# Optimization experiments

Measured on AMD Instinct MI355X. Metric: run time of the kernel, lower is better.

The kernel has to match this reference:

```python
import jax, jax.numpy as jnp
import numpy as np

B, CIN, COUT, H, W = 8, 128, 128, 64, 64

# kernel-grid base offsets (dy, dx), row-major k = kh*3 + kw, matching torch base_offset-1
BASE = jnp.array([[-1, -1], [-1, 0], [-1, 1],
                  [0, -1], [0, 0], [0, 1],
                  [1, -1], [1, 0], [1, 1]], dtype=jnp.float32)  # [9,2]
CORNER = jnp.array([1, 0, 1, 0, 0, 0, 1, 0, 1], dtype=jnp.float32)  # mask1 per kernel tap
EDGE = jnp.array([0, 1, 0, 1, 0, 1, 0, 1, 0], dtype=jnp.float32)    # mask2 per kernel tap


def conv3x3(x, w, b=None):
    out = jax.lax.conv_general_dilated(
        x, w, window_strides=(1, 1), padding=((1, 1), (1, 1)),
        dimension_numbers=('NCHW', 'OIHW', 'NCHW'))
    if b is not None:
        out = out + b[None, :, None, None]
    return out


def bilinear_sample(x, py, px):
    Bv, C, Hin, Win = x.shape
    y0 = jnp.floor(py)
    x0 = jnp.floor(px)
    wy = py - y0
    wx = px - x0
    y0i = y0.astype(jnp.int32)
    x0i = x0.astype(jnp.int32)
    xf = x.reshape(Bv, C, Hin * Win)

    def corner(yi, xi):
        valid = ((yi >= 0) & (yi < Hin) & (xi >= 0) & (xi < Win)).astype(x.dtype)
        idx = jnp.clip(yi, 0, Hin - 1) * Win + jnp.clip(xi, 0, Win - 1)  # [B,K,Ho,Wo]
        g = jax.vmap(lambda xb, ib: xb[:, ib])(xf, idx)  # [B,C,K,Ho,Wo]
        return g * valid[:, None]

    v00 = corner(y0i, x0i)
    v01 = corner(y0i, x0i + 1)
    v10 = corner(y0i + 1, x0i)
    v11 = corner(y0i + 1, x0i + 1)
    wy = wy[:, None]
    wx = wx[:, None]
    return (v00 * (1 - wy) * (1 - wx) + v01 * (1 - wy) * wx
            + v10 * wy * (1 - wx) + v11 * wy * wx)


def setup_inputs() -> dict:
    key = jax.random.key(0)
    k1, k2, k3 = jax.random.split(key, 3)
    x = jax.random.normal(k1, (B, CIN, H, W), dtype=jnp.float32)
    # small offset-conv weights keep predicted offsets in a realistic sub-pixel range
    w_off = jax.random.normal(k2, (5, CIN, 3, 3), dtype=jnp.float32) * 0.02
    b_off = jnp.zeros((5,), dtype=jnp.float32)
    w = jax.random.normal(k3, (COUT, CIN, 3, 3), dtype=jnp.float32) * (1.0 / np.sqrt(CIN * 9))
    b = jnp.zeros((COUT,), dtype=jnp.float32)
    return {"x": x, "w_off": w_off, "b_off": b_off, "w": w, "b": b}


def reference(x, w_off, b_off, w, b):
    off = conv3x3(x, w_off, b_off)          # [B,5,H,W]
    scale1 = jax.nn.relu(off[:, 2:3]) + 1.0  # corner scale [B,1,H,W]
    scale2 = jax.nn.relu(off[:, 3:4]) + 1.0  # edge scale   [B,1,H,W]
    shift = off[:, :2]                       # equivariant shift vector [B,2,H,W]

    # per-tap scale; center tap gets 0 but its base offset is (0,0) anyway
    scale_k = CORNER[None, :, None, None] * scale1 + EDGE[None, :, None, None] * scale2  # [B,9,H,W]
    # deform offset = scaled_base - base + shift = base*(scale-1) + shift
    delta = BASE[None, :, :, None, None] * (scale_k - 1.0)[:, :, None] + shift[:, None]  # [B,9,2,H,W]

    hs = jnp.arange(H, dtype=x.dtype)
    ws = jnp.arange(W, dtype=x.dtype)
    # sampling positions: p0 + base_k + offset_k (stride=1, pad=1)
    py = hs[None, None, :, None] + BASE[None, :, 0, None, None] + delta[:, :, 0]  # [B,9,H,W]
    px = ws[None, None, None, :] + BASE[None, :, 1, None, None] + delta[:, :, 1]

    sampled = bilinear_sample(x, py, px)  # [B,CIN,9,H,W]
    out = jnp.einsum('bckhw,ock->bohw', sampled, w.reshape(COUT, CIN, 9))
    return out + b[None, :, None, None]
```

## Files before the change

kernel.cpp:

```cpp
#include <hip/hip_runtime.h>

#define Wd 64
#define Hd 64
#define HWp 4096
#define CIN_ 128
#define COUT_ 128

typedef _Float16 f16;
typedef _Float16 h2    __attribute__((ext_vector_type(2)));
typedef _Float16 f16x8 __attribute__((ext_vector_type(8)));
typedef float f32x4    __attribute__((ext_vector_type(4)));

__device__ inline ushort f2h(float f) {
    f16 h = (f16)f;
    return __builtin_bit_cast(ushort, h);
}
__device__ inline h2 gb(const int4& g, int d) {
    return __builtin_bit_cast(h2, (&g.x)[d]);
}
__device__ inline h2 dup(float f) {
    f16 h = (f16)f;
    h2 r; r[0] = h; r[1] = h;
    return r;
}
struct H8 { h2 r[4]; };

__global__ __launch_bounds__(512) void prep_offsets_kernel(
    const float* __restrict__ x, const float* __restrict__ w,
    const float* __restrict__ w_off, const float* __restrict__ b_off,
    ushort* __restrict__ xt, ushort* __restrict__ w_t2,
    float4* __restrict__ der)
{
    __shared__ char smem[43520];
    int blk = blockIdx.x;
    int t = threadIdx.x;

    if (blk < 40) {
        int i8 = blk * 512 + t;
        if (i8 < 18432) {
            int lane = i8 & 63;
            int ii   = (i8 >> 6) & 3;
            int wm   = (i8 >> 8) & 1;
            int s    = i8 >> 9;
            int o  = wm * 64 + ii * 16 + (lane & 15);
            int cb = (s & 3) * 32 + (lane >> 4) * 8;
            int k  = s >> 2;
            ushort tmp[8];
            #pragma unroll
            for (int j = 0; j < 8; j++)
                tmp[j] = f2h(w[o * 1152 + (cb + j) * 9 + k]);
            *(int4*)&w_t2[(size_t)i8 * 8] = *(int4*)tmp;
        }
    } else {
        float* wl    = (float*)smem;
        float* part  = (float*)(smem + 18432);
        ushort* tile = (ushort*)(smem + 26624);
        int blk2 = blk - 40;
        int b = blk2 & 7;
        int h = blk2 >> 3;

        for (int i = t; i < 4608; i += 512) {
            int j = i / 1152;
            int r = i - j * 1152;
            wl[r * 4 + j] = w_off[i];
        }
        __syncthreads();

        int pi = t & 63, cg = t >> 6;
        const float* xb = x + (size_t)(b * CIN_ + cg * 16) * HWp;

        int idxc[3];
        float mskl[3], mskc[3], mskr[3];
        #pragma unroll
        for (int dy = 0; dy < 3; dy++) {
            int hy = h + dy - 1;
            int hyc = min(max(hy, 0), Hd - 1);
            bool vr = (hy >= 0) && (hy < Hd);
            idxc[dy] = hyc * Wd + pi;
            mskc[dy] = vr ? 1.0f : 0.0f;
            mskl[dy] = (vr && pi > 0) ? 1.0f : 0.0f;
            mskr[dy] = (vr && pi < Wd - 1) ? 1.0f : 0.0f;
        }

        float o0 = 0.f, o1 = 0.f, o2 = 0.f, o3 = 0.f;
        #pragma unroll
        for (int c4 = 0; c4 < 4; c4++) {
            ushort4 hv;
            #pragma unroll
            for (int j = 0; j < 4; j++) {
                int c = c4 * 4 + j;
                const float* xp = xb + c * HWp;
                const float* wc = &wl[(cg * 16 + c) * 36];
                float xv[9];
                #pragma unroll
                for (int dy = 0; dy < 3; dy++) {
                    float v = xp[idxc[dy]];
                    xv[dy * 3 + 0] = __shfl_up(v, 1) * mskl[dy];
                    xv[dy * 3 + 1] = v * mskc[dy];
                    xv[dy * 3 + 2] = __shfl_down(v, 1) * mskr[dy];
                }
                (&hv.x)[j] = f2h(xv[4]);
                #pragma unroll
                for (int tp = 0; tp < 9; tp++) {
                    float4 wj = *(const float4*)&wc[tp * 4];
                    o0 += xv[tp] * wj.x; o1 += xv[tp] * wj.y;
                    o2 += xv[tp] * wj.z; o3 += xv[tp] * wj.w;
                }
            }
            *(ushort4*)&tile[pi * 132 + cg * 16 + c4 * 4] = hv;
        }
        part[t * 4 + 0] = o0;
        part[t * 4 + 1] = o1;
        part[t * 4 + 2] = o2;
        part[t * 4 + 3] = o3;
        __syncthreads();

        {
            ushort* dst = xt + ((size_t)b * HWp + h * 64) * CIN_;
            #pragma unroll
            for (int k = 0; k < 2; k++) {
                int q = t + k * 512;
                int row = q >> 4, c16 = q & 15;
                int4 v = *(const int4*)&tile[row * 132 + c16 * 8];
                *(int4*)(dst + q * 8) = v;
            }
        }

        if (t < 64) {
            float s0 = b_off[0], s1 = b_off[1], s2 = b_off[2], s3 = b_off[3];
            #pragma unroll
            for (int q = 0; q < 8; q++) {
                s0 += part[(q * 64 + t) * 4 + 0];
                s1 += part[(q * 64 + t) * 4 + 1];
                s2 += part[(q * 64 + t) * 4 + 2];
                s3 += part[(q * 64 + t) * 4 + 3];
            }
            float4 d;
            d.x = s0;
            d.y = s1;
            d.z = fmaxf(s2, 0.f) + 1.f;
            d.w = fmaxf(s3, 0.f) + 1.f;
            der[(size_t)b * HWp + h * Wd + t] = d;
        }
    }
}

__global__ __launch_bounds__(256, 2) void deform_gemm_mfma(
    const ushort* __restrict__ xt, const ushort* __restrict__ w_t2,
    const float* __restrict__ bias, const float4* __restrict__ der,
    float* __restrict__ out)
{
    __shared__ ushort A_lds[2][2][4096];
    __shared__ ushort S_lds[2][2][64 * 40];
    __shared__ int4 MI[9][64];
    __shared__ int4 MW[9][64];

    int t = threadIdx.x;
    int b = blockIdx.x & 7;
    int rp = blockIdx.x >> 3;
    int p0 = rp << 6;
    const char* xtb = (const char*)(xt + (size_t)b * HWp * CIN_);

    int p  = t >> 2;
    int c8 = (t & 3) << 3;
    int c8b = c8 * 2;

    int wv = t >> 6, lane = t & 63;
    int wm = wv & 1, ns = wv >> 1;
    int lm = lane & 15, lq = lane >> 4;

    f32x4 acc[4][2] = {};

    {
        int pg = p0 + p;
        float fh = (float)(pg >> 6), fp = (float)(pg & 63);
        float4 dv = der[(size_t)b * HWp + pg];
        for (int k = (t & 3); k < 9; k += 4) {
            int ky = (k * 11) >> 5;
            int kx = k - ky * 3;
            float by = (float)(ky - 1), bx = (float)(kx - 1);
            bool corner = (ky != 1) && (kx != 1);
            bool edge = (ky != 1) ^ (kx != 1);
            float sk = corner ? dv.z : (edge ? dv.w : 0.0f);
            float py = fh + by * sk + dv.x;
            float px = fp + bx * sk + dv.y;
            float y0f = floorf(py), x0f = floorf(px);
            float wy = py - y0f, wx = px - x0f;
            int y0 = (int)y0f, x0 = (int)x0f;
            int y1 = y0 + 1, x1 = x0 + 1;
            float vy0 = (y0 >= 0 && y0 < Hd) ? 1.f : 0.f;
            float vy1 = (y1 >= 0 && y1 < Hd) ? 1.f : 0.f;
            float vx0 = (x0 >= 0 && x0 < Wd) ? 1.f : 0.f;
            float vx1 = (x1 >= 0 && x1 < Wd) ? 1.f : 0.f;
            int cy0 = min(max(y0, 0), Hd - 1), cy1 = min(max(y1, 0), Hd - 1);
            int cx0 = min(max(x0, 0), Wd - 1), cx1 = min(max(x1, 0), Wd - 1);
            int4 ii;
            ii.x = (cy0 * Wd + cx0) << 8;
            ii.y = (cy0 * Wd + cx1) << 8;
            ii.z = (cy1 * Wd + cx0) << 8;
            ii.w = (cy1 * Wd + cx1) << 8;
            MI[k][p] = ii;
            H8 hw;
            hw.r[0] = dup((1.f - wy) * (1.f - wx) * vy0 * vx0);
            hw.r[1] = dup((1.f - wy) * wx * vy0 * vx1);
            hw.r[2] = dup(wy * (1.f - wx) * vy1 * vx0);
            hw.r[3] = dup(wy * wx * vy1 * vx1);
            MW[k][p] = __builtin_bit_cast(int4, hw);
        }
    }
    __syncthreads();

    int vo0, vo1, vo2, vo3;

    auto stageA = [&](int buf, int st) {
        const ushort* src = w_t2 + (size_t)st * 8192;
        #pragma unroll
        for (int cc = 0; cc < 2; cc++) {
            #pragma unroll
            for (int hrow = 0; hrow < 2; hrow++) {
                const ushort* g = src + cc * 4096 + (wv * 2 + hrow) * 512 + lane * 8;
                ushort* l = &A_lds[buf][cc][(wv * 2 + hrow) * 512];
                __builtin_amdgcn_global_load_lds(
                    (const __attribute__((address_space(1))) unsigned int*)g,
                    (__attribute__((address_space(3))) unsigned int*)l, 16, 0, 0);
            }
        }
    };

    auto issue = [&](int st, int4 (&G)[2][4]) {
        #pragma unroll
        for (int cc = 0; cc < 2; cc++) {
            int q = (2 * st + cc) & 3;
            G[cc][0] = *(const int4*)(xtb + (vo0 + q * 64));
            G[cc][1] = *(const int4*)(xtb + (vo1 + q * 64));
            G[cc][2] = *(const int4*)(xtb + (vo2 + q * 64));
            G[cc][3] = *(const int4*)(xtb + (vo3 + q * 64));
        }
    };
    auto commitS = [&](int buf, const int4 (&G)[2][4], const H8& cw) {
        #pragma unroll
        for (int cc = 0; cc < 2; cc++) {
            H8 tmp;
            #pragma unroll
            for (int d = 0; d < 4; d++) {
                h2 r = gb(G[cc][0], d) * cw.r[0];
                r = gb(G[cc][1], d) * cw.r[1] + r;
                r = gb(G[cc][2], d) * cw.r[2] + r;
                r = gb(G[cc][3], d) * cw.r[3] + r;
                tmp.r[d] = r;
            }
            *(int4*)&S_lds[buf][cc][p * 40 + c8] = __builtin_bit_cast(int4, tmp);
        }
    };
    auto mfmaSec = [&](int cur) {
        #pragma unroll
        for (int cc = 0; cc < 2; cc++) {
            f16x8 af[4], bfr[2];
            #pragma unroll
            for (int i = 0; i < 4; i++)
                af[i] = *(const f16x8*)&A_lds[cur][cc][(wm * 4 + i) * 512 + lane * 8];
            #pragma unroll
            for (int f = 0; f < 2; f++)
                bfr[f] = *(const f16x8*)&S_lds[cur][cc][(ns * 32 + f * 16 + lm) * 40 + lq * 8];
            #pragma unroll
            for (int i = 0; i < 4; i++)
                #pragma unroll
                for (int f = 0; f < 2; f++)
                    acc[i][f] = __builtin_amdgcn_mfma_f32_16x16x32_f16(
                        af[i], bfr[f], acc[i][f], 0, 0, 0);
        }
    };

    int4 GA[2][4], GB[2][4];
    H8 cwA, cwB;
    int4 idxN;

    stageA(0, 0);
    __builtin_amdgcn_sched_barrier(0);
    {
        int4 i0 = MI[0][p];
        vo0 = i0.x + c8b; vo1 = i0.y + c8b; vo2 = i0.z + c8b; vo3 = i0.w + c8b;
    }
    issue(0, GA);
    cwA = __builtin_bit_cast(H8, MW[0][p]);
    commitS(0, GA, cwA);
    issue(1, GB);
    idxN = MI[1][p];
    asm volatile("s_waitcnt vmcnt(8) lgkmcnt(0)" ::: "memory");
    __builtin_amdgcn_s_barrier();
    __builtin_amdgcn_sched_barrier(0);

#define BODY(ST, GC, GI, CWC, CWR, DORD)                                     \
    {                                                                        \
        int cur_ = (ST) & 1, nb_ = cur_ ^ 1;                                 \
        if ((ST) + 1 < 18) stageA(nb_, (ST) + 1);                            \
        __builtin_amdgcn_sched_barrier(0);                                   \
        if ((ST) + 2 < 18) {                                                 \
            if (DORD) {                                                      \
                vo0 = idxN.x + c8b; vo1 = idxN.y + c8b;                      \
                vo2 = idxN.z + c8b; vo3 = idxN.w + c8b;                      \
            }                                                                \
            issue((ST) + 2, GI);                                             \
        }                                                                    \
        if (DORD) {                                                          \
            idxN = MI[min(((ST) >> 1) + 2, 8)][p];                           \
            CWR = __builtin_bit_cast(H8, MW[min(((ST) >> 1) + 1, 8)][p]);    \
        }                                                                    \
        __builtin_amdgcn_s_setprio(1);                                       \
        mfmaSec(cur_);                                                       \
        __builtin_amdgcn_s_setprio(0);                                       \
        if ((ST) + 1 < 18) commitS(nb_, GC, CWC);                            \
        if ((ST) + 2 < 18) {                                                 \
            asm volatile("s_waitcnt vmcnt(8) lgkmcnt(0)" ::: "memory");      \
        } else {                                                             \
            asm volatile("s_waitcnt vmcnt(0) lgkmcnt(0)" ::: "memory");      \
        }                                                                    \
        __builtin_amdgcn_s_barrier();                                        \
        __builtin_amdgcn_sched_barrier(0);                                   \
    }

    for (int su = 0; su < 4; su++) {
        int st = su << 2;
        BODY(st,     GB, GA, cwA, cwB, 1);
        BODY(st + 1, GA, GB, cwB, cwB, 0);
        BODY(st + 2, GB, GA, cwB, cwA, 1);
        BODY(st + 3, GA, GB, cwA, cwA, 0);
    }
    BODY(16, GB, GA, cwA, cwB, 1);
    BODY(17, GA, GB, cwB, cwB, 0);
#undef BODY

    #pragma unroll
    for (int i = 0; i < 4; i++) {
        #pragma unroll
        for (int r = 0; r < 4; r++) {
            int o = wm * 64 + i * 16 + lq * 4 + r;
            float bv = bias[o];
            float* orow = out + (size_t)(b * COUT_ + o) * HWp + p0 + ns * 32 + lm;
            #pragma unroll
            for (int f = 0; f < 2; f++)
                __builtin_nontemporal_store(acc[i][f][r] + bv, &orow[f * 16]);
        }
    }
}

extern "C" void kernel_launch(void* const* d_in, const int* in_sizes, int n_in,
                              void* d_out, int out_size, void* d_ws, size_t ws_size,
                              hipStream_t stream) {
    const float* x     = (const float*)d_in[0];
    const float* w_off = (const float*)d_in[1];
    const float* b_off = (const float*)d_in[2];
    const float* w     = (const float*)d_in[3];
    const float* bias  = (const float*)d_in[4];
    float* out = (float*)d_out;

    char* ws = (char*)d_ws;
    ushort* xt   = (ushort*)ws;
    ushort* w_t2 = (ushort*)(ws + 8388608);
    float4* der  = (float4*)(ws + 8683520);

    prep_offsets_kernel<<<552, 512, 0, stream>>>(x, w, w_off, b_off,
                                                 xt, w_t2, der);
    deform_gemm_mfma<<<512, 256, 0, stream>>>(xt, w_t2, bias, der, out);
}
```

Measured before the change: 110.4 us.

## Fuse offset prep and deformable GEMM into one kernel with grid barrier

Merges the prep/offset kernel and the MFMA deformable GEMM into a single persistent launch of 512 blocks. Each block computes its own row's offsets, fp16 transposed input slice and a share of the weight conversion, then keeps the offsets in LDS instead of a global buffer. A global atomic-counter barrier makes every block wait until all xt and w_t2 data is written before the GEMM phase starts. This removes one launch and the der round trip through memory. It risks deadlock if not all 512 blocks are co-resident, has a spin timeout, and adds a memset call.

```diff
diff --git a/kernel.cpp b/kernel.cpp
--- a/kernel.cpp
+++ b/kernel.cpp
@@ -25,19 +25,31 @@
 }
 struct H8 { h2 r[4]; };
 
-__global__ __launch_bounds__(512) void prep_offsets_kernel(
+__global__ __launch_bounds__(256, 2) void fused_deform(
     const float* __restrict__ x, const float* __restrict__ w,
     const float* __restrict__ w_off, const float* __restrict__ b_off,
+    const float* __restrict__ bias,
     ushort* __restrict__ xt, ushort* __restrict__ w_t2,
-    float4* __restrict__ der)
+    unsigned* __restrict__ flag, float* __restrict__ out)
 {
-    __shared__ char smem[43520];
-    int blk = blockIdx.x;
+    __shared__ ushort A_lds[2][2][4096];
+    __shared__ ushort S_lds[2][2][64 * 40];
+    __shared__ int4 MI[9][64];
+    __shared__ int4 MW[9][64];
+    __shared__ float4 derL[64];
+
     int t = threadIdx.x;
-
-    if (blk < 40) {
-        int i8 = blk * 512 + t;
-        if (i8 < 18432) {
+    int b = blockIdx.x & 7;
+    int hq = blockIdx.x >> 3;
+
+    {
+        char* base = (char*)&A_lds[0][0][0];
+        float* wl    = (float*)base;
+        float* part  = (float*)(base + 18432);
+        ushort* tile = (ushort*)(base + 22528);
+
+        if (t < 36) {
+            int i8 = blockIdx.x * 36 + t;
             int lane = i8 & 63;
             int ii   = (i8 >> 6) & 3;
             int wm   = (i8 >> 8) & 1;
@@ -51,23 +63,17 @@
                 tmp[j] = f2h(w[o * 1152 + (cb + j) * 9 + k]);
             *(int4*)&w_t2[(size_t)i8 * 8] = *(int4*)tmp;
         }
-    } else {
-        float* wl    = (float*)smem;
-        float* part  = (float*)(smem + 18432);
-        ushort* tile = (ushort*)(smem + 26624);
-        int blk2 = blk - 40;
-        int b = blk2 & 7;
-        int h = blk2 >> 3;
-
-        for (int i = t; i < 4608; i += 512) {
+
+        for (int i = t; i < 4608; i += 256) {
             int j = i / 1152;
             int r = i - j * 1152;
             wl[r * 4 + j] = w_off[i];
         }
         __syncthreads();
 
-        int pi = t & 63, cg = t >> 6;
-        const float* xb = x + (size_t)(b * CIN_ + cg * 16) * HWp;
+        int pi = t & 63, cg4 = t >> 6;
+        int h = hq;
+        const float* xb = x + (size_t)(b * CIN_ + cg4 * 32) * HWp;
 
         int idxc[3];
         float mskl[3], mskc[3], mskr[3];
@@ -83,14 +89,14 @@
         }
 
         float o0 = 0.f, o1 = 0.f, o2 = 0.f, o3 = 0.f;
-        #pragma unroll
-        for (int c4 = 0; c4 < 4; c4++) {
+        #pragma unroll 2
+        for (int c4 = 0; c4 < 8; c4++) {
             ushort4 hv;
             #pragma unroll
             for (int j = 0; j < 4; j++) {
                 int c = c4 * 4 + j;
                 const float* xp = xb + c * HWp;
-                const float* wc = &wl[(cg * 16 + c) * 36];
+                const float* wc = &wl[(cg4 * 32 + c) * 36];
                 float xv[9];
                 #pragma unroll
                 for (int dy = 0; dy < 3; dy++) {
@@ -107,7 +113,7 @@
                     o2 += xv[tp] * wj.z; o3 += xv[tp] * wj.w;
                 }
             }
-            *(ushort4*)&tile[pi * 132 + cg * 16 + c4 * 4] = hv;
+            *(ushort4*)&tile[pi * 132 + cg4 * 32 + c4 * 4] = hv;
         }
         part[t * 4 + 0] = o0;
         part[t * 4 + 1] = o1;
@@ -118,8 +124,8 @@
         {
             ushort* dst = xt + ((size_t)b * HWp + h * 64) * CIN_;
             #pragma unroll
-            for (int k = 0; k < 2; k++) {
-                int q = t + k * 512;
+            for (int k = 0; k < 4; k++) {
+                int q = t + k * 256;
                 int row = q >> 4, c16 = q & 15;
                 int4 v = *(const int4*)&tile[row * 132 + c16 * 8];
                 *(int4*)(dst + q * 8) = v;
@@ -129,7 +135,7 @@
         if (t < 64) {
             float s0 = b_off[0], s1 = b_off[1], s2 = b_off[2], s3 = b_off[3];
             #pragma unroll
-            for (int q = 0; q < 8; q++) {
+            for (int q = 0; q < 4; q++) {
                 s0 += part[(q * 64 + t) * 4 + 0];
                 s1 += part[(q * 64 + t) * 4 + 1];
                 s2 += part[(q * 64 + t) * 4 + 2];
@@ -140,25 +146,67 @@
             d.y = s1;
             d.z = fmaxf(s2, 0.f) + 1.f;
             d.w = fmaxf(s3, 0.f) + 1.f;
-            der[(size_t)b * HWp + h * Wd + t] = d;
-        }
-    }
-}
-
-__global__ __launch_bounds__(256, 2) void deform_gemm_mfma(
-    const ushort* __restrict__ xt, const ushort* __restrict__ w_t2,
-    const float* __restrict__ bias, const float4* __restrict__ der,
-    float* __restrict__ out)
-{
-    __shared__ ushort A_lds[2][2][4096];
-    __shared__ ushort S_lds[2][2][64 * 40];
-    __shared__ int4 MI[9][64];
-    __shared__ int4 MW[9][64];
-
-    int t = threadIdx.x;
-    int b = blockIdx.x & 7;
-    int rp = blockIdx.x >> 3;
-    int p0 = rp << 6;
+            derL[t] = d;
+        }
+        __syncthreads();
+
+        {
+            int p = t >> 2;
+            int pg = hq * 64 + p;
+            float fh = (float)(pg >> 6), fp = (float)(pg & 63);
+            float4 dv = derL[p];
+            for (int k = (t & 3); k < 9; k += 4) {
+                int ky = (k * 11) >> 5;
+                int kx = k - ky * 3;
+                float by = (float)(ky - 1), bx = (float)(kx - 1);
+                bool corner = (ky != 1) && (kx != 1);
+                bool edge = (ky != 1) ^ (kx != 1);
+                float sk = corner ? dv.z : (edge ? dv.w : 0.0f);
+                float py = fh + by * sk + dv.x;
+                float px = fp + bx * sk + dv.y;
+                float y0f = floorf(py), x0f = floorf(px);
+                float wy = py - y0f, wx = px - x0f;
+                int y0 = (int)y0f, x0 = (int)x0f;
+                int y1 = y0 + 1, x1 = x0 + 1;
+                float vy0 = (y0 >= 0 && y0 < Hd) ? 1.f : 0.f;
+                float vy1 = (y1 >= 0 && y1 < Hd) ? 1.f : 0.f;
+                float vx0 = (x0 >= 0 && x0 < Wd) ? 1.f : 0.f;
+                float vx1 = (x1 >= 0 && x1 < Wd) ? 1.f : 0.f;
+                int cy0 = min(max(y0, 0), Hd - 1), cy1 = min(max(y1, 0), Hd - 1);
+                int cx0 = min(max(x0, 0), Wd - 1), cx1 = min(max(x1, 0), Wd - 1);
+                int4 ii;
+                ii.x = (cy0 * Wd + cx0) << 8;
+                ii.y = (cy0 * Wd + cx1) << 8;
+                ii.z = (cy1 * Wd + cx0) << 8;
+                ii.w = (cy1 * Wd + cx1) << 8;
+                MI[k][p] = ii;
+                H8 hw;
+                hw.r[0] = dup((1.f - wy) * (1.f - wx) * vy0 * vx0);
+                hw.r[1] = dup((1.f - wy) * wx * vy0 * vx1);
+                hw.r[2] = dup(wy * (1.f - wx) * vy1 * vx0);
+                hw.r[3] = dup(wy * wx * vy1 * vx1);
+                MW[k][p] = __builtin_bit_cast(int4, hw);
+            }
+        }
+    }
+
+    __syncthreads();
+    if (t == 0) {
+        __threadfence();
+        atomicAdd(flag, 1u);
+        unsigned v;
+        long tries = 0;
+        do {
+            v = __hip_atomic_load(flag, __ATOMIC_RELAXED,
+                                  __HIP_MEMORY_SCOPE_AGENT);
+            if (++tries > (1L << 26)) break;
+            __builtin_amdgcn_s_sleep(8);
+        } while (v < 512u);
+    }
+    __syncthreads();
+    __threadfence();
+
+    int p0 = hq << 6;
     const char* xtb = (const char*)(xt + (size_t)b * HWp * CIN_);
 
     int p  = t >> 2;
@@ -170,45 +218,6 @@
     int lm = lane & 15, lq = lane >> 4;
 
     f32x4 acc[4][2] = {};
-
-    {
-        int pg = p0 + p;
-        float fh = (float)(pg >> 6), fp = (float)(pg & 63);
-        float4 dv = der[(size_t)b * HWp + pg];
-        for (int k = (t & 3); k < 9; k += 4) {
-            int ky = (k * 11) >> 5;
-            int kx = k - ky * 3;
-            float by = (float)(ky - 1), bx = (float)(kx - 1);
-            bool corner = (ky != 1) && (kx != 1);
-            bool edge = (ky != 1) ^ (kx != 1);
-            float sk = corner ? dv.z : (edge ? dv.w : 0.0f);
-            float py = fh + by * sk + dv.x;
-            float px = fp + bx * sk + dv.y;
-            float y0f = floorf(py), x0f = floorf(px);
-            float wy = py - y0f, wx = px - x0f;
-            int y0 = (int)y0f, x0 = (int)x0f;
-            int y1 = y0 + 1, x1 = x0 + 1;
-            float vy0 = (y0 >= 0 && y0 < Hd) ? 1.f : 0.f;
-            float vy1 = (y1 >= 0 && y1 < Hd) ? 1.f : 0.f;
-            float vx0 = (x0 >= 0 && x0 < Wd) ? 1.f : 0.f;
-            float vx1 = (x1 >= 0 && x1 < Wd) ? 1.f : 0.f;
-            int cy0 = min(max(y0, 0), Hd - 1), cy1 = min(max(y1, 0), Hd - 1);
-            int cx0 = min(max(x0, 0), Wd - 1), cx1 = min(max(x1, 0), Wd - 1);
-            int4 ii;
-            ii.x = (cy0 * Wd + cx0) << 8;
-            ii.y = (cy0 * Wd + cx1) << 8;
-            ii.z = (cy1 * Wd + cx0) << 8;
-            ii.w = (cy1 * Wd + cx1) << 8;
-            MI[k][p] = ii;
-            H8 hw;
-            hw.r[0] = dup((1.f - wy) * (1.f - wx) * vy0 * vx0);
-            hw.r[1] = dup((1.f - wy) * wx * vy0 * vx1);
-            hw.r[2] = dup(wy * (1.f - wx) * vy1 * vx0);
-            hw.r[3] = dup(wy * wx * vy1 * vx1);
-            MW[k][p] = __builtin_bit_cast(int4, hw);
-        }
-    }
-    __syncthreads();
 
     int vo0, vo1, vo2, vo3;
 
@@ -355,11 +364,11 @@
     float* out = (float*)d_out;
 
     char* ws = (char*)d_ws;
-    ushort* xt   = (ushort*)ws;
-    ushort* w_t2 = (ushort*)(ws + 8388608);
-    float4* der  = (float4*)(ws + 8683520);
-
-    prep_offsets_kernel<<<552, 512, 0, stream>>>(x, w, w_off, b_off,
-                                                 xt, w_t2, der);
-    deform_gemm_mfma<<<512, 256, 0, stream>>>(xt, w_t2, bias, der, out);
-}
+    ushort* xt    = (ushort*)ws;
+    ushort* w_t2  = (ushort*)(ws + 8388608);
+    unsigned* flag = (unsigned*)(ws + 8683520);
+
+    hipMemsetAsync(flag, 0, 4, stream);
+    fused_deform<<<512, 256, 0, stream>>>(x, w, w_off, b_off, bias,
+                                          xt, w_t2, flag, out);
+}
```

After: 187.3 us. 1.7x slower.
